# Kernel tuning notes

Hardware: AMD Instinct MI355X
Metric: run time of the kernel (lower is better)

Reference implementation:

```python
import jax, jax.numpy as jnp
import numpy as np

B, H, W, C, F, K = 64, 56, 56, 256, 256, 3


def _conv(x, w, padding):
    # NHWC input, HWIO kernel, stride 1
    return jax.lax.conv_general_dilated(
        x, w, window_strides=(1, 1), padding=padding,
        dimension_numbers=('NHWC', 'HWIO', 'NHWC'))


def setup_inputs() -> dict:
    key = jax.random.key(0)
    kx, kw = jax.random.split(key)
    x = jax.random.normal(kx, (B, H, W, C), dtype=jnp.float32)
    stdv = 1.0 / np.sqrt(K * K * C)  # matches build()'s init scale
    w = (jax.random.normal(kw, (K, K, C, F), dtype=jnp.float32) * stdv).astype(jnp.float32)
    return {"x": x, "w": w}


def reference(x, w):
    # fp16_grad forward: round-trip weights through fp16
    wq = w.astype(jnp.float16).astype(jnp.float32)
    # binarize_weight forward value: sign(clip(w, -1, 1))
    wb = jnp.sign(jnp.clip(wq, -1.0, 1.0))
    return _conv(x, wb, 'SAME')
```

## Files before the change

kernel.cpp:

```cpp
#include <hip/hip_runtime.h>
#include <hip/hip_bf16.h>
#include <hip/hip_fp16.h>

typedef __bf16 bf16x8 __attribute__((ext_vector_type(8)));
typedef float  f32x4  __attribute__((ext_vector_type(4)));

#define C_H 56
#define C_W 56
#define C_C 256
#define C_F 256
#define C_B 64
#define N_PIX (C_B * C_H * C_W)
#define WB_ELEMS (9 * C_C * C_F)
#define WB_BYTES (WB_ELEMS * 2)
#define ZBUF_BYTES 1024
#define XB_OFF (WB_BYTES + ZBUF_BYTES)
#define X_ELEMS (N_PIX * C_C)

#define GLOAD_LDS16(g, l)                                                   \
    __builtin_amdgcn_global_load_lds(                                        \
        (const __attribute__((address_space(1))) void*)(g),                  \
        (__attribute__((address_space(3))) void*)(l), 16, 0, 0)

__global__ void prep_w_kernel(const float* __restrict__ w, __bf16* __restrict__ wbT) {
    int idx = blockIdx.x * 256 + threadIdx.x;
    int f = idx & 255;
    int c = (idx >> 8) & 255;
    int s = idx >> 16;
    float wf = w[idx];
    float v = __half2float(__float2half(wf));
    float sgn = (v > 0.f) ? 1.f : ((v < 0.f) ? -1.f : 0.f);
    wbT[(s << 16) + (f << 8) + c] = (__bf16)sgn;
}

__global__ void zero_kernel(float* __restrict__ z) {
    z[threadIdx.x] = 0.f;
}

__global__ void prep_x_kernel(const float* __restrict__ x, __bf16* __restrict__ xb) {
    int i = blockIdx.x * 256 + threadIdx.x;
    const f32x4* p = reinterpret_cast<const f32x4*>(x) + (size_t)i * 2;
    f32x4 a = p[0], b = p[1];
    bf16x8 o;
    o[0] = (__bf16)a[0]; o[1] = (__bf16)a[1]; o[2] = (__bf16)a[2]; o[3] = (__bf16)a[3];
    o[4] = (__bf16)b[0]; o[5] = (__bf16)b[1]; o[6] = (__bf16)b[2]; o[7] = (__bf16)b[3];
    reinterpret_cast<bf16x8*>(xb)[i] = o;
}

__global__ __launch_bounds__(512, 2) void conv_mfma8_kernel(
    const char* __restrict__ xbp,
    const char* __restrict__ wbp,
    const char* __restrict__ zp,
    float* __restrict__ out) {

    __shared__ __align__(16) char sm[4][32768];

    const int nbid = (blockIdx.x & 7) * 98 + (blockIdx.x >> 3);
    const long m0 = (long)nbid * 256;

    const int tid  = threadIdx.x;
    const int lane = tid & 63;
    const int wave = tid >> 6;
    const int l15  = lane & 15;
    const int g4   = lane >> 4;
    const int wm   = wave >> 2;
    const int wn   = wave & 3;
    const int colr = ((g4 ^ ((l15 >> 1) & 3)) << 4);
    const int rdA = (wm * 128 + l15) * 64 + colr;
    const int rdB = 16384 + (wn * 64 + l15) * 64 + colr;

    const int r0 = tid >> 2;
    const int sw = ((tid & 3) ^ ((r0 >> 1) & 3)) << 4;
    const int p0 = (int)m0 + r0;
    const int p1 = p0 + 128;
    const int rem0 = p0 % 3136;
    const int rem1 = p1 % 3136;
    const int y0 = rem0 / 56, x0 = rem0 - (rem0 / 56) * 56;
    const int y1 = rem1 / 56, x1 = rem1 - (rem1 / 56) * 56;

    auto stage = [&](int kt) {
        int cc = (kt * 57) >> 9;
        int s  = kt - 9 * cc;
        int s3 = (s * 171) >> 9;
        int dy = s3 - 1;
        int dx = s - 3 * s3 - 1;
        int doff = dy * 56 + dx;
        size_t cb = (size_t)(cc << 6) + sw;
        bool v0 = ((unsigned)(y0 + dy) < 56u) & ((unsigned)(x0 + dx) < 56u);
        bool v1 = ((unsigned)(y1 + dy) < 56u) & ((unsigned)(x1 + dx) < 56u);
        const char* a0 = v0 ? xbp + (size_t)(p0 + doff) * 512 + cb : zp + sw;
        const char* a1 = v1 ? xbp + (size_t)(p1 + doff) * 512 + cb : zp + sw;
        const char* b0 = wbp + (size_t)((s << 8) + r0) * 512 + cb;
        const char* b1 = wbp + (size_t)((s << 8) + r0 + 128) * 512 + cb;
        char* L = &sm[kt & 3][0];
        GLOAD_LDS16(a0, L + tid * 16);
        GLOAD_LDS16(a1, L + 8192 + tid * 16);
        GLOAD_LDS16(b0, L + 16384 + tid * 16);
        GLOAD_LDS16(b1, L + 24576 + tid * 16);
    };

    f32x4 acc[8][4];
#pragma unroll
    for (int i = 0; i < 8; ++i)
#pragma unroll
        for (int j = 0; j < 4; ++j)
            acc[i][j] = (f32x4){0.f, 0.f, 0.f, 0.f};

    bf16x8 Af[8], Bx[4], By[4];

    auto body = [&](int t, bf16x8 (&Bc)[4], bf16x8 (&Bn)[4], bool doStage, bool doPre) {
        __builtin_amdgcn_s_barrier();
        __builtin_amdgcn_sched_barrier(0);
        if (doStage) stage(t + 3);
        const char* L1 = &sm[(t + 1) & 3][0];
        const char* Ab = L1 + rdA;
        const char* Bb = L1 + rdB;
        __builtin_amdgcn_s_setprio(1);
#pragma unroll
        for (int ai = 0; ai < 8; ++ai) {
#pragma unroll
            for (int bj = 0; bj < 4; ++bj)
                acc[ai][bj] = __builtin_amdgcn_mfma_f32_16x16x32_bf16(
                    Af[ai], Bc[bj], acc[ai][bj], 0, 0, 0);
            if (doPre)
                Af[ai] = *reinterpret_cast<const bf16x8*>(Ab + ai * 1024);
        }
        __builtin_amdgcn_s_setprio(0);
        if (doPre) {
#pragma unroll
            for (int bj = 0; bj < 4; ++bj)
                Bn[bj] = *reinterpret_cast<const bf16x8*>(Bb + bj * 1024);
            asm volatile("s_waitcnt lgkmcnt(12)" ::: "memory");
            __builtin_amdgcn_sched_barrier(0);
        }
    };

    stage(0); stage(1); stage(2);
    asm volatile("s_waitcnt vmcnt(8)" ::: "memory");
    __builtin_amdgcn_s_barrier();
    __builtin_amdgcn_sched_barrier(0);
    {
        const char* L0 = &sm[0][0];
#pragma unroll
        for (int ai = 0; ai < 8; ++ai)
            Af[ai] = *reinterpret_cast<const bf16x8*>(L0 + rdA + ai * 1024);
#pragma unroll
        for (int bj = 0; bj < 4; ++bj)
            Bx[bj] = *reinterpret_cast<const bf16x8*>(L0 + rdB + bj * 1024);
    }
    asm volatile("s_waitcnt lgkmcnt(0)" ::: "memory");
    __builtin_amdgcn_sched_barrier(0);

    for (int tt = 0; tt < 68; tt += 2) {
        asm volatile("s_waitcnt vmcnt(4)" ::: "memory");
        body(tt, Bx, By, true, true);
        asm volatile("s_waitcnt vmcnt(4)" ::: "memory");
        body(tt + 1, By, Bx, true, true);
    }
    asm volatile("s_waitcnt vmcnt(4)" ::: "memory");
    body(68, Bx, By, true, true);
    asm volatile("s_waitcnt vmcnt(4)" ::: "memory");
    body(69, By, Bx, false, true);
    asm volatile("s_waitcnt vmcnt(0)" ::: "memory");
    body(70, Bx, By, false, true);
    body(71, By, Bx, false, false);

#pragma unroll
    for (int ai = 0; ai < 8; ++ai) {
#pragma unroll
        for (int j = 0; j < 4; ++j) {
            long row = m0 + wm * 128 + ai * 16 + g4 * 4 + j;
            float* op = out + row * C_F + wn * 64 + l15;
#pragma unroll
            for (int bj = 0; bj < 4; ++bj)
                op[bj * 16] = acc[ai][bj][j];
        }
    }
}

__global__ __launch_bounds__(256) void conv_fallback_kernel(
    const float* __restrict__ xf,
    const __bf16* __restrict__ wbT, const char* __restrict__ zbuf,
    float* __restrict__ out) {

    const int lane = threadIdx.x & 63;
    const int wave = threadIdx.x >> 6;
    const int l15  = lane & 15;
    const int g    = lane >> 4;
    const int goff = g * 8;
    const long m0  = (long)blockIdx.x * 64;
    const int fbase = wave * 64;

    int ry[4], rx[4];
    long rbase[4];
#pragma unroll
    for (int ai = 0; ai < 4; ++ai) {
        int rr = (int)m0 + ai * 16 + l15;
        int b = rr / 3136;
        int rem = rr - b * 3136;
        int yy2 = rem / 56;
        ry[ai] = yy2;
        rx[ai] = rem - yy2 * 56;
        rbase[ai] = (long)rr * C_C;
    }

    f32x4 acc[4][4];
#pragma unroll
    for (int i = 0; i < 4; ++i)
#pragma unroll
        for (int j = 0; j < 4; ++j)
            acc[i][j] = (f32x4){0.f, 0.f, 0.f, 0.f};

    for (int s = 0; s < 9; ++s) {
        const int dy = s / 3 - 1;
        const int dx = (s - (s / 3) * 3) - 1;
        const float* af[4];
#pragma unroll
        for (int ai = 0; ai < 4; ++ai) {
            bool v = ((unsigned)(ry[ai] + dy) < 56u) & ((unsigned)(rx[ai] + dx) < 56u);
            long off = rbase[ai] + (long)(dy * C_W + dx) * C_C + goff;
            af[ai] = v ? (xf + off) : ((const float*)zbuf + goff);
        }
        const __bf16* bp = wbT + ((size_t)(s * 256 + fbase + l15)) * C_C + goff;

#pragma unroll
        for (int cc = 0; cc < 8; ++cc) {
            const int c0 = cc * 32;
            bf16x8 A[4], Bf[4];
#pragma unroll
            for (int ai = 0; ai < 4; ++ai) {
                const f32x4* p = reinterpret_cast<const f32x4*>(af[ai] + c0);
                f32x4 u = p[0], w2 = p[1];
                bf16x8 t;
                t[0] = (__bf16)u[0]; t[1] = (__bf16)u[1]; t[2] = (__bf16)u[2]; t[3] = (__bf16)u[3];
                t[4] = (__bf16)w2[0]; t[5] = (__bf16)w2[1]; t[6] = (__bf16)w2[2]; t[7] = (__bf16)w2[3];
                A[ai] = t;
            }
#pragma unroll
            for (int bj = 0; bj < 4; ++bj)
                Bf[bj] = *reinterpret_cast<const bf16x8*>(bp + bj * 16 * C_C + c0);
#pragma unroll
            for (int ai = 0; ai < 4; ++ai)
#pragma unroll
                for (int bj = 0; bj < 4; ++bj)
                    acc[ai][bj] = __builtin_amdgcn_mfma_f32_16x16x32_bf16(A[ai], Bf[bj], acc[ai][bj], 0, 0, 0);
        }
    }

#pragma unroll
    for (int ai = 0; ai < 4; ++ai) {
#pragma unroll
        for (int j = 0; j < 4; ++j) {
            long row = m0 + ai * 16 + g * 4 + j;
            float* op = out + row * C_F + fbase + l15;
#pragma unroll
            for (int bj = 0; bj < 4; ++bj)
                op[bj * 16] = acc[ai][bj][j];
        }
    }
}

extern "C" void kernel_launch(void* const* d_in, const int* in_sizes, int n_in,
                              void* d_out, int out_size, void* d_ws, size_t ws_size,
                              hipStream_t stream) {
    const float* x = (const float*)d_in[0];
    const float* w = (const float*)d_in[1];
    float* out = (float*)d_out;

    char* ws = (char*)d_ws;
    __bf16* wbT = (__bf16*)ws;
    char* zbuf = ws + WB_BYTES;
    __bf16* xb = (__bf16*)(ws + XB_OFF);

    const bool prex = ws_size >= (size_t)XB_OFF + (size_t)X_ELEMS * 2;

    prep_w_kernel<<<WB_ELEMS / 256, 256, 0, stream>>>(w, wbT);
    zero_kernel<<<1, 256, 0, stream>>>((float*)zbuf);

    if (prex) {
        prep_x_kernel<<<X_ELEMS / 8 / 256, 256, 0, stream>>>(x, xb);
        conv_mfma8_kernel<<<N_PIX / 256, 512, 0, stream>>>(
            (const char*)xb, (const char*)wbT, zbuf, out);
    } else {
        conv_fallback_kernel<<<N_PIX / 64, 256, 0, stream>>>(x, wbT, zbuf, out);
    }
}
```

Baseline: 319.4 us.

## Split each k-tile into two ping-pong phases with barrier-synchronized LDS reads

Restructures the main GEMM loop so each k-tile runs as two half-phases. Each phase loads half the A fragments (plus B in the first phase), issues half of the next stage's global-to-LDS copies, then runs 16 MFMAs with all LDS reads completed. This replaces the register-prefetch scheme that overlapped LDS reads with MFMAs and used 8 A fragments, which cuts register pressure and spreads global loads more evenly. The cost is two barriers per phase and a full lgkmcnt(0) wait before the MFMAs, which exposes LDS latency unless other waves fill the gap.

```diff
diff --git a/kernel.cpp b/kernel.cpp
--- a/kernel.cpp
+++ b/kernel.cpp
@@ -78,25 +78,28 @@
     const int y0 = rem0 / 56, x0 = rem0 - (rem0 / 56) * 56;
     const int y1 = rem1 / 56, x1 = rem1 - (rem1 / 56) * 56;
 
-    auto stage = [&](int kt) {
+    auto stage_half = [&](int kt, int abHalf) {
         int cc = (kt * 57) >> 9;
         int s  = kt - 9 * cc;
-        int s3 = (s * 171) >> 9;
-        int dy = s3 - 1;
-        int dx = s - 3 * s3 - 1;
-        int doff = dy * 56 + dx;
+        char* L = &sm[kt & 3][0];
         size_t cb = (size_t)(cc << 6) + sw;
-        bool v0 = ((unsigned)(y0 + dy) < 56u) & ((unsigned)(x0 + dx) < 56u);
-        bool v1 = ((unsigned)(y1 + dy) < 56u) & ((unsigned)(x1 + dx) < 56u);
-        const char* a0 = v0 ? xbp + (size_t)(p0 + doff) * 512 + cb : zp + sw;
-        const char* a1 = v1 ? xbp + (size_t)(p1 + doff) * 512 + cb : zp + sw;
-        const char* b0 = wbp + (size_t)((s << 8) + r0) * 512 + cb;
-        const char* b1 = wbp + (size_t)((s << 8) + r0 + 128) * 512 + cb;
-        char* L = &sm[kt & 3][0];
-        GLOAD_LDS16(a0, L + tid * 16);
-        GLOAD_LDS16(a1, L + 8192 + tid * 16);
-        GLOAD_LDS16(b0, L + 16384 + tid * 16);
-        GLOAD_LDS16(b1, L + 24576 + tid * 16);
+        if (abHalf == 0) {
+            int s3 = (s * 171) >> 9;
+            int dy = s3 - 1;
+            int dx = s - 3 * s3 - 1;
+            int doff = dy * 56 + dx;
+            bool v0 = ((unsigned)(y0 + dy) < 56u) & ((unsigned)(x0 + dx) < 56u);
+            bool v1 = ((unsigned)(y1 + dy) < 56u) & ((unsigned)(x1 + dx) < 56u);
+            const char* a0 = v0 ? xbp + (size_t)(p0 + doff) * 512 + cb : zp + sw;
+            const char* a1 = v1 ? xbp + (size_t)(p1 + doff) * 512 + cb : zp + sw;
+            GLOAD_LDS16(a0, L + tid * 16);
+            GLOAD_LDS16(a1, L + 8192 + tid * 16);
+        } else {
+            const char* b0 = wbp + (size_t)((s << 8) + r0) * 512 + cb;
+            const char* b1 = wbp + (size_t)((s << 8) + r0 + 128) * 512 + cb;
+            GLOAD_LDS16(b0, L + 16384 + tid * 16);
+            GLOAD_LDS16(b1, L + 24576 + tid * 16);
+        }
     };
 
     f32x4 acc[8][4];
@@ -106,64 +109,59 @@
         for (int j = 0; j < 4; ++j)
             acc[i][j] = (f32x4){0.f, 0.f, 0.f, 0.f};
 
-    bf16x8 Af[8], Bx[4], By[4];
-
-    auto body = [&](int t, bf16x8 (&Bc)[4], bf16x8 (&Bn)[4], bool doStage, bool doPre) {
-        __builtin_amdgcn_s_barrier();
-        __builtin_amdgcn_sched_barrier(0);
-        if (doStage) stage(t + 3);
-        const char* L1 = &sm[(t + 1) & 3][0];
-        const char* Ab = L1 + rdA;
-        const char* Bb = L1 + rdB;
-        __builtin_amdgcn_s_setprio(1);
-#pragma unroll
-        for (int ai = 0; ai < 8; ++ai) {
-#pragma unroll
-            for (int bj = 0; bj < 4; ++bj)
-                acc[ai][bj] = __builtin_amdgcn_mfma_f32_16x16x32_bf16(
-                    Af[ai], Bc[bj], acc[ai][bj], 0, 0, 0);
-            if (doPre)
-                Af[ai] = *reinterpret_cast<const bf16x8*>(Ab + ai * 1024);
-        }
-        __builtin_amdgcn_s_setprio(0);
-        if (doPre) {
-#pragma unroll
-            for (int bj = 0; bj < 4; ++bj)
-                Bn[bj] = *reinterpret_cast<const bf16x8*>(Bb + bj * 1024);
-            asm volatile("s_waitcnt lgkmcnt(12)" ::: "memory");
-            __builtin_amdgcn_sched_barrier(0);
-        }
-    };
-
-    stage(0); stage(1); stage(2);
-    asm volatile("s_waitcnt vmcnt(8)" ::: "memory");
+    bf16x8 Af[4], Bf[4];
+
+#define VM8 asm volatile("s_waitcnt vmcnt(8)" ::: "memory")
+#define VM4 asm volatile("s_waitcnt vmcnt(4)" ::: "memory")
+#define VM0 asm volatile("s_waitcnt vmcnt(0)" ::: "memory")
+
+#define PHASE(Q, H, DOSTAGE, TAILWAIT)                                      \
+    {                                                                        \
+        const char* Lb = &sm[(Q)][0];                                        \
+        if ((H) == 0) {                                                      \
+            _Pragma("unroll")                                                \
+            for (int bj = 0; bj < 4; ++bj)                                   \
+                Bf[bj] = *reinterpret_cast<const bf16x8*>(Lb + rdB + bj * 1024); \
+        }                                                                    \
+        _Pragma("unroll")                                                    \
+        for (int ai = 0; ai < 4; ++ai)                                       \
+            Af[ai] = *reinterpret_cast<const bf16x8*>(Lb + rdA + ((H) * 4 + ai) * 1024); \
+        if (DOSTAGE) stage_half(kt + 3, (H));                                \
+        __builtin_amdgcn_s_barrier();                                        \
+        asm volatile("s_waitcnt lgkmcnt(0)" ::: "memory");                   \
+        __builtin_amdgcn_sched_barrier(0);                                   \
+        __builtin_amdgcn_s_setprio(1);                                       \
+        _Pragma("unroll")                                                    \
+        for (int ai = 0; ai < 4; ++ai)                                       \
+            _Pragma("unroll")                                                \
+            for (int bj = 0; bj < 4; ++bj)                                   \
+                acc[(H) * 4 + ai][bj] = __builtin_amdgcn_mfma_f32_16x16x32_bf16( \
+                    Af[ai], Bf[bj], acc[(H) * 4 + ai][bj], 0, 0, 0);         \
+        __builtin_amdgcn_s_setprio(0);                                       \
+        __builtin_amdgcn_sched_barrier(0);                                   \
+        TAILWAIT;                                                            \
+        __builtin_amdgcn_s_barrier();                                        \
+    }
+
+    stage_half(0, 0); stage_half(0, 1);
+    stage_half(1, 0); stage_half(1, 1);
+    stage_half(2, 0); stage_half(2, 1);
+    VM8;
     __builtin_amdgcn_s_barrier();
-    __builtin_amdgcn_sched_barrier(0);
-    {
-        const char* L0 = &sm[0][0];
-#pragma unroll
-        for (int ai = 0; ai < 8; ++ai)
-            Af[ai] = *reinterpret_cast<const bf16x8*>(L0 + rdA + ai * 1024);
-#pragma unroll
-        for (int bj = 0; bj < 4; ++bj)
-            Bx[bj] = *reinterpret_cast<const bf16x8*>(L0 + rdB + bj * 1024);
-    }
-    asm volatile("s_waitcnt lgkmcnt(0)" ::: "memory");
-    __builtin_amdgcn_sched_barrier(0);
-
-    for (int tt = 0; tt < 68; tt += 2) {
-        asm volatile("s_waitcnt vmcnt(4)" ::: "memory");
-        body(tt, Bx, By, true, true);
-        asm volatile("s_waitcnt vmcnt(4)" ::: "memory");
-        body(tt + 1, By, Bx, true, true);
-    }
-    asm volatile("s_waitcnt vmcnt(4)" ::: "memory");
-    body(68, Bx, By, true, true);
-    asm volatile("s_waitcnt vmcnt(4)" ::: "memory");
-    body(69, By, Bx, false, true);
-    asm volatile("s_waitcnt vmcnt(0)" ::: "memory");
-    body(70, Bx, By, false, true);
-    body(71, By, Bx, false, false);
+
+    for (int it = 0; it < 17; ++it) {
+        int kt;
+        kt = it * 4 + 0; PHASE(0, 0, true, ); PHASE(0, 1, true, VM8);
+        kt = it * 4 + 1; PHASE(1, 0, true, ); PHASE(1, 1, true, VM8);
+        kt = it * 4 + 2; PHASE(2, 0, true, ); PHASE(2, 1, true, VM8);
+        kt = it * 4 + 3; PHASE(3, 0, true, ); PHASE(3, 1, true, VM8);
+    }
+    { int kt = 68; PHASE(0, 0, true,  ); PHASE(0, 1, true,  VM8); }
+    { int kt = 69; PHASE(1, 0, false, ); PHASE(1, 1, false, VM4); }
+    { int kt = 70; PHASE(2, 0, false, ); PHASE(2, 1, false, VM0); }
+    { int kt = 71; PHASE(3, 0, false, ); PHASE(3, 1, false, ); }
+
+#undef PHASE
 
 #pragma unroll
     for (int ai = 0; ai < 8; ++ai) {
```

Measured after the change: 340.7 us. 6.7% more time.
